# Kernel tuning notes

Measured on AMD Instinct MI355X. Metric: run time of the kernel, lower is better.

## Reference

```python
import jax, jax.numpy as jnp
import numpy as np
from jax import lax

D_MODEL = 512
N_BLOCKS = 8
VOCAB = 2048
MEL = 80
D_INNER = 2 * D_MODEL      # standard Mamba expand=2
STATE = 16                 # AudioConstants.MAMBA_STATE_DIM
DT_RANK = D_MODEL // 16    # 32
CONV_K = 4                 # causal depthwise conv kernel
B, T = 4, 2048


def setup_inputs() -> dict:
    key = jax.random.key(0)
    ks = jax.random.split(key, 16)
    s = 0.02
    nb = N_BLOCKS
    inp = {
        "feats": jax.random.normal(ks[0], (B, T, MEL), jnp.float32),
        "feat_lens": jax.random.randint(ks[1], (B,), 0, T, jnp.int32),
        # frontend
        "conv1_w": jax.random.normal(ks[2], (D_MODEL, MEL, 3), jnp.float32) * s,
        "conv1_b": jnp.zeros((D_MODEL,), jnp.float32),
        "conv2_w": jax.random.normal(ks[3], (D_MODEL, D_MODEL, 3), jnp.float32) * s,
        "conv2_b": jnp.zeros((D_MODEL,), jnp.float32),
        # stacked per-block Mamba params (leading dim = n_blocks)
        "norm_w": jnp.ones((nb, D_MODEL), jnp.float32),
        "in_proj_w": jax.random.normal(ks[4], (nb, D_MODEL, 2 * D_INNER), jnp.float32) * s,
        "dwconv_w": jax.random.normal(ks[5], (nb, D_INNER, CONV_K), jnp.float32) * s,
        "dwconv_b": jnp.zeros((nb, D_INNER), jnp.float32),
        "x_proj_w": jax.random.normal(ks[6], (nb, D_INNER, DT_RANK + 2 * STATE), jnp.float32) * s,
        "dt_proj_w": jax.random.normal(ks[7], (nb, DT_RANK, D_INNER), jnp.float32) * s,
        "dt_proj_b": jnp.full((nb, D_INNER), -4.6, jnp.float32),  # softplus(-4.6)~0.01
        "A_log": jnp.tile(jnp.log(jnp.arange(1, STATE + 1, dtype=jnp.float32))[None, None, :], (nb, D_INNER, 1)),
        "Dskip": jnp.ones((nb, D_INNER), jnp.float32),
        "out_proj_w": jax.random.normal(ks[8], (nb, D_INNER, D_MODEL), jnp.float32) * s,
        # CTC head
        "head_w": jax.random.normal(ks[9], (D_MODEL, VOCAB), jnp.float32) * s,
        "head_b": jnp.zeros((VOCAB,), jnp.float32),
    }
    return inp


def _conv1d(x, w, b, stride, pad):
    # x: (B, Cin, L), w: (Cout, Cin, K)
    y = lax.conv_general_dilated(x, w, (stride,), [(pad, pad)],
                                 dimension_numbers=("NCH", "OIH", "NCH"))
    return y + b[None, :, None]


def _mamba_layer(x, p):
    nw, ipw, cw, cb, xpw, dpw, dpb, alog, dsk, opw = p
    res = x
    # RMSNorm
    xn = x * lax.rsqrt(jnp.mean(x * x, axis=-1, keepdims=True) + 1e-5) * nw
    xz = xn @ ipw                                # (B, L, 2*di)
    xs, z = jnp.split(xz, 2, axis=-1)
    # causal depthwise conv over time
    xc = jnp.pad(xs.transpose(0, 2, 1), ((0, 0), (0, 0), (CONV_K - 1, 0)))
    xc = lax.conv_general_dilated(xc, cw[:, None, :], (1,), [(0, 0)],
                                  dimension_numbers=("NCH", "OIH", "NCH"),
                                  feature_group_count=D_INNER)
    xs = jax.nn.silu((xc + cb[None, :, None]).transpose(0, 2, 1))  # (B, L, di)
    # input-dependent SSM params
    xdb = xs @ xpw                               # (B, L, dt_rank + 2N)
    dt, Bm, Cm = jnp.split(xdb, [DT_RANK, DT_RANK + STATE], axis=-1)
    delta = jax.nn.softplus(dt @ dpw + dpb)      # (B, L, di)
    A = -jnp.exp(alog)                           # (di, N)
    dA = jnp.exp(delta[..., None] * A)           # (B, L, di, N)
    dBx = delta[..., None] * Bm[:, :, None, :] * xs[..., None]

    def step(h, inp):
        dA_t, dBx_t, C_t = inp                   # (B,di,N),(B,di,N),(B,N)
        h = dA_t * h + dBx_t
        y = jnp.einsum("bdn,bn->bd", h, C_t)
        return h, y

    h0 = jnp.zeros((x.shape[0], D_INNER, STATE), x.dtype)
    _, ys = lax.scan(step, h0, (dA.transpose(1, 0, 2, 3),
                                dBx.transpose(1, 0, 2, 3),
                                Cm.transpose(1, 0, 2)))
    y = ys.transpose(1, 0, 2) + xs * dsk          # (B, L, di)
    y = y * jax.nn.silu(z)
    return res + y @ opw, None


def reference(feats, feat_lens, conv1_w, conv1_b, conv2_w, conv2_b,
              norm_w, in_proj_w, dwconv_w, dwconv_b, x_proj_w,
              dt_proj_w, dt_proj_b, A_log, Dskip, out_proj_w,
              head_w, head_b):
    x = feats.transpose(0, 2, 1)                  # (B, 80, T)
    x = jax.nn.gelu(_conv1d(x, conv1_w, conv1_b, 2, 1), approximate=False)
    x = jax.nn.gelu(_conv1d(x, conv2_w, conv2_b, 2, 1), approximate=False)
    x = x.transpose(0, 2, 1)                      # (B, T/4, D)
    params = (norm_w, in_proj_w, dwconv_w, dwconv_b, x_proj_w,
              dt_proj_w, dt_proj_b, A_log, Dskip, out_proj_w)
    x, _ = lax.scan(_mamba_layer, x, params)
    logits = x @ head_w + head_b                  # (B, T/4, V)
    out_lens = jnp.maximum(feat_lens // 4, 1)
    return logits, out_lens
```

## Files before the change

kernel.cpp:

```cpp
#include <hip/hip_runtime.h>
#include <hip/hip_bf16.h>

#define DMODEL 512
#define NB 8
#define VOCABSZ 2048
#define MEL 80
#define DIN 1024
#define NSTATE 16
#define BATCH 4
#define TIN 2048
#define LL1 1024
#define LSEQ 512
#define MROWS (BATCH*LSEQ)
#define M1ROWS (BATCH*LL1)
#define NCHUNK 16
#define LCHUNK 32

typedef unsigned short u16;
typedef unsigned int   u32;
typedef __attribute__((ext_vector_type(8))) short short8;
typedef __attribute__((ext_vector_type(4))) float f32x4;

__device__ __forceinline__ float bf2f(u16 v) { return __uint_as_float(((u32)v) << 16); }
__device__ __forceinline__ u16 f2bf(float f) {
    u32 u = __float_as_uint(f);
    return (u16)((u + 0x7fffu + ((u >> 16) & 1u)) >> 16);
}
__device__ __forceinline__ float gelu_exact(float v) {
    return 0.5f * v * (1.0f + erff(v * 0.70710678118654752f));
}
__device__ __forceinline__ float silu_f(float v) { return v / (1.0f + __expf(-v)); }
__device__ __forceinline__ float softplus_f(float v) { return v > 20.f ? v : log1pf(__expf(v)); }

template<int WM, int WN, int MR, int NR, int EPI, int SPLITK>
__global__ __launch_bounds__(WM*WN*64) void gemm2_bf16(
    const u16* __restrict__ A, int lda,
    const u16* __restrict__ BT, int ldb,
    const float* __restrict__ bias,
    float* __restrict__ Cf, u16* __restrict__ Cb, int ldc,
    int K, int zstride)
{
    constexpr int BM = WM * MR * 16;
    constexpr int BN = WN * NR * 16;
    constexpr int NT = WM * WN * 64;
    constexpr int LA = (BM * 4) / NT;
    constexpr int LB = (BN * 4) / NT;
    __shared__ __align__(16) u16 As[2][BM * 32];
    __shared__ __align__(16) u16 Bs[2][BN * 32];
    const int tid = threadIdx.x;
    const int m0 = blockIdx.y * BM, n0 = blockIdx.x * BN;
    const int lane = tid & 63;
    const int wave = tid >> 6;
    const int wm = wave / WN, wn = wave % WN;
    const int lr = lane & 15, lk = lane >> 4;

    int kt0 = 0, kend = K;
    if (SPLITK > 1) {
        const int kb = K / SPLITK;
        kt0 = blockIdx.z * kb;
        kend = kt0 + kb;
        Cf += (size_t)blockIdx.z * zstride;
    }

    f32x4 acc[MR][NR];
#pragma unroll
    for (int m = 0; m < MR; ++m)
#pragma unroll
        for (int n = 0; n < NR; ++n) acc[m][n] = (f32x4){0.f, 0.f, 0.f, 0.f};

    auto stage = [&](int buf, int kt) {
#pragma unroll
        for (int c = 0; c < LA; ++c) {
            int idx = c * NT + tid;
            const u16* src = A + (size_t)(m0 + (idx >> 2)) * lda + kt + (idx & 3) * 8;
            __builtin_amdgcn_global_load_lds(
                (const __attribute__((address_space(1))) void*)src,
                (__attribute__((address_space(3))) void*)&As[buf][idx * 8], 16, 0, 0);
        }
#pragma unroll
        for (int c = 0; c < LB; ++c) {
            int idx = c * NT + tid;
            const u16* src = BT + (size_t)(n0 + (idx >> 2)) * ldb + kt + (idx & 3) * 8;
            __builtin_amdgcn_global_load_lds(
                (const __attribute__((address_space(1))) void*)src,
                (__attribute__((address_space(3))) void*)&Bs[buf][idx * 8], 16, 0, 0);
        }
    };

    stage(0, kt0);
    __syncthreads();
    int cur = 0;
    for (int kt = kt0; kt < kend; kt += 32) {
        if (kt + 32 < kend) stage(cur ^ 1, kt + 32);
        short8 a[MR], b[NR];
#pragma unroll
        for (int m = 0; m < MR; ++m)
            a[m] = *(const short8*)&As[cur][((wm * MR + m) * 16 + lr) * 32 + lk * 8];
#pragma unroll
        for (int n = 0; n < NR; ++n)
            b[n] = *(const short8*)&Bs[cur][((wn * NR + n) * 16 + lr) * 32 + lk * 8];
#pragma unroll
        for (int m = 0; m < MR; ++m)
#pragma unroll
            for (int n = 0; n < NR; ++n)
                acc[m][n] = __builtin_amdgcn_mfma_f32_16x16x32_bf16(a[m], b[n], acc[m][n], 0, 0, 0);
        __syncthreads();
        cur ^= 1;
    }

#pragma unroll
    for (int m = 0; m < MR; ++m) {
#pragma unroll
        for (int n = 0; n < NR; ++n) {
#pragma unroll
            for (int r = 0; r < 4; ++r) {
                const int row = m0 + (wm * MR + m) * 16 + lk * 4 + r;
                const int col = n0 + (wn * NR + n) * 16 + lr;
                float v = acc[m][n][r];
                if (EPI == 1)      v += bias[col];
                else if (EPI == 2) v = gelu_exact(v + bias[col]);
                else if (EPI == 3) v = softplus_f(v + bias[col]);
                else if (EPI == 4) v += Cf[(size_t)row * ldc + col];
                else if (EPI == 6) v *= bias[row];
                if (Cf) Cf[(size_t)row * ldc + col] = v;
                if (Cb) Cb[(size_t)row * ldc + col] = f2bf(v);
            }
        }
    }
}

__global__ __launch_bounds__(256) void tcast_k(const float* __restrict__ in, u16* __restrict__ out,
                                               int R, int C, size_t sin, size_t sout) {
    in  += (size_t)blockIdx.z * sin;
    out += (size_t)blockIdx.z * sout;
    __shared__ float s[32][33];
    const int tx = threadIdx.x & 31, ty = threadIdx.x >> 5;
    const int r0 = blockIdx.y * 32, c0 = blockIdx.x * 32;
#pragma unroll
    for (int i = 0; i < 4; ++i)
        s[ty + i * 8][tx] = in[(size_t)(r0 + ty + i * 8) * C + c0 + tx];
    __syncthreads();
#pragma unroll
    for (int i = 0; i < 4; ++i)
        out[(size_t)(c0 + ty + i * 8) * R + r0 + tx] = f2bf(s[tx][ty + i * 8]);
}

__global__ __launch_bounds__(256) void tcast_nw_k(const float* __restrict__ in, u16* __restrict__ out,
                                                  const float* __restrict__ nwp,
                                                  int R, int C, size_t sin, size_t sout, int nws) {
    in  += (size_t)blockIdx.z * sin;
    out += (size_t)blockIdx.z * sout;
    nwp += (size_t)blockIdx.z * nws;
    __shared__ float s[32][33];
    const int tx = threadIdx.x & 31, ty = threadIdx.x >> 5;
    const int r0 = blockIdx.y * 32, c0 = blockIdx.x * 32;
#pragma unroll
    for (int i = 0; i < 4; ++i)
        s[ty + i * 8][tx] = in[(size_t)(r0 + ty + i * 8) * C + c0 + tx];
    __syncthreads();
    const float nwv = nwp[r0 + tx];
#pragma unroll
    for (int i = 0; i < 4; ++i)
        out[(size_t)(c0 + ty + i * 8) * R + r0 + tx] = f2bf(s[tx][ty + i * 8] * nwv);
}

__global__ void castpad_k(const float* __restrict__ in, u16* __restrict__ out,
                          int rows, int cin, int cout, int instride,
                          size_t sin, size_t sout) {
    in  += (size_t)blockIdx.z * sin;
    out += (size_t)blockIdx.z * sout;
    int idx = blockIdx.x * 256 + threadIdx.x;
    if (idx >= rows * cout) return;
    int c = idx % cout, r = idx / cout;
    out[idx] = (c < cin) ? f2bf(in[(size_t)r * instride + c]) : (u16)0;
}

__global__ void im2col1_k(const float* __restrict__ feats, u16* __restrict__ out,
                          const int* __restrict__ feat_lens, float* __restrict__ lens_out) {
    int idx = blockIdx.x * 256 + threadIdx.x;
    if (blockIdx.x == 0 && threadIdx.x < BATCH) {
        int v = feat_lens[threadIdx.x] / 4;
        if (v < 1) v = 1;
        lens_out[threadIdx.x] = (float)v;
    }
    int c = idx & 255, m = idx >> 8;
    int l1 = m & (LL1 - 1), b = m >> 10;
    float v = 0.f;
    if (c < 240) {
        int ci = c / 3, kk = c - ci * 3;
        int t = 2 * l1 - 1 + kk;
        if (t >= 0 && t < TIN) v = feats[((size_t)b * TIN + t) * MEL + ci];
    }
    out[idx] = f2bf(v);
}

__global__ void im2col2_k(const u16* __restrict__ y1b, u16* __restrict__ out) {
    int idx = blockIdx.x * 256 + threadIdx.x;
    int c = idx % 1536, m = idx / 1536;
    int l = m & (LSEQ - 1), b = m >> 9;
    int ci = c / 3, kk = c - ci * 3;
    int t = 2 * l - 1 + kk;
    out[idx] = (t >= 0 && t < LL1) ? y1b[((size_t)b * LL1 + t) * 512 + ci] : (u16)0;
}

__global__ __launch_bounds__(256) void rowsc_k(const float* __restrict__ X,
                                               float* __restrict__ scrow) {
    const int lane = threadIdx.x & 63;
    const int row = blockIdx.x * 4 + (threadIdx.x >> 6);
    const float4 v0 = *(const float4*)&X[(size_t)row * 512 + lane * 8];
    const float4 v1 = *(const float4*)&X[(size_t)row * 512 + lane * 8 + 4];
    float ss = v0.x * v0.x + v0.y * v0.y + v0.z * v0.z + v0.w * v0.w
             + v1.x * v1.x + v1.y * v1.y + v1.z * v1.z + v1.w * v1.w;
#pragma unroll
    for (int o = 1; o < 64; o <<= 1) ss += __shfl_xor(ss, o);
    if (lane == 0) scrow[row] = rsqrtf(ss * (1.f / 512.f) + 1e-5f);
}

__global__ __launch_bounds__(256) void dwconv_silu_k(const u16* __restrict__ xzb,
                                                     const float* __restrict__ cw,
                                                     const float* __restrict__ cb,
                                                     u16* __restrict__ xsb) {
    int d = blockIdx.x * 256 + threadIdx.x;
    int m = blockIdx.y;
    int l = m & (LSEQ - 1);
    int b = m >> 9;
    float acc = cb[d];
    const float4 w4 = *reinterpret_cast<const float4*>(&cw[d * 4]);
    const float wk[4] = {w4.x, w4.y, w4.z, w4.w};
#pragma unroll
    for (int k = 0; k < 4; k++) {
        int t = l - 3 + k;
        if (t >= 0) acc += wk[k] * bf2f(xzb[((size_t)(b * LSEQ + t)) * (2 * DIN) + d]);
    }
    xsb[(size_t)m * DIN + d] = f2bf(silu_f(acc));
}

__global__ __launch_bounds__(256) void dtproj_k(
    const float* __restrict__ part, const u16* __restrict__ dpwT,
    const float* __restrict__ dpb, u16* __restrict__ delb)
{
    __shared__ __align__(16) u16 As[128 * 32];
    __shared__ __align__(16) u16 Bs[64 * 32];
    const int tid = threadIdx.x;
    const int m0 = blockIdx.y * 128, n0 = blockIdx.x * 64;
    {
        const int r = tid >> 1, hh = (tid & 1) * 16;
        const size_t o = (size_t)(m0 + r) * 64 + hh;
        float4 s[4];
#pragma unroll
        for (int q = 0; q < 4; ++q) {
            s[q] = *(const float4*)&part[o + q * 4];
#pragma unroll
            for (int p = 1; p < 4; ++p) {
                const float4 v = *(const float4*)&part[(size_t)p * 131072 + o + q * 4];
                s[q].x += v.x; s[q].y += v.y; s[q].z += v.z; s[q].w += v.w;
            }
        }
        u32 pk[8];
#pragma unroll
        for (int q = 0; q < 4; ++q) {
            pk[2 * q]     = (u32)f2bf(s[q].x) | ((u32)f2bf(s[q].y) << 16);
            pk[2 * q + 1] = (u32)f2bf(s[q].z) | ((u32)f2bf(s[q].w) << 16);
        }
        *(uint4*)&As[r * 32 + hh]     = make_uint4(pk[0], pk[1], pk[2], pk[3]);
        *(uint4*)&As[r * 32 + hh + 8] = make_uint4(pk[4], pk[5], pk[6], pk[7]);
    }
    {
        const int row = tid >> 2, p4 = (tid & 3) * 8;
        const u16* src = dpwT + (size_t)(n0 + row) * 32 + p4;
        __builtin_amdgcn_global_load_lds(
            (const __attribute__((address_space(1))) void*)src,
            (__attribute__((address_space(3))) void*)&Bs[row * 32 + p4], 16, 0, 0);
    }
    __syncthreads();
    const int lane = tid & 63, wave = tid >> 6;
    const int wm = wave >> 1, wn = wave & 1;
    const int lr = lane & 15, lk = lane >> 4;
    short8 b8[2];
#pragma unroll
    for (int n = 0; n < 2; ++n)
        b8[n] = *(const short8*)&Bs[((wn * 2 + n) * 16 + lr) * 32 + lk * 8];
#pragma unroll
    for (int m = 0; m < 4; ++m) {
        const short8 a8 = *(const short8*)&As[((wm * 4 + m) * 16 + lr) * 32 + lk * 8];
#pragma unroll
        for (int n = 0; n < 2; ++n) {
            f32x4 acc = __builtin_amdgcn_mfma_f32_16x16x32_bf16(a8, b8[n], (f32x4){0.f,0.f,0.f,0.f}, 0, 0, 0);
#pragma unroll
            for (int r = 0; r < 4; ++r) {
                const int row = m0 + (wm * 4 + m) * 16 + lk * 4 + r;
                const int col = n0 + (wn * 2 + n) * 16 + lr;
                delb[(size_t)row * DIN + col] = f2bf(softplus_f(acc[r] + dpb[col]));
            }
        }
    }
}

template<int PASS>
__global__ __launch_bounds__(256) void scan_chunk_k(
    const u16* __restrict__ deltab, const u16* __restrict__ xsb,
    const float* __restrict__ part, const u16* __restrict__ xzb,
    const float* __restrict__ alog, const float* __restrict__ dsk,
    float* __restrict__ P, float* __restrict__ Q,
    u16* __restrict__ yb)
{
    __shared__ float s_bc[LCHUNK * 32];
    __shared__ float s_dl[LCHUNK * 64];
    __shared__ float s_xs[LCHUNK * 64];
    __shared__ float s_z [PASS ? LCHUNK * 64 : 1];

    const int tid  = threadIdx.x;
    const int j    = tid & 3;
    const int dsub = tid >> 2;
    const int d0   = blockIdx.x * 64;
    const int c    = blockIdx.y;
    const int b    = blockIdx.z;
    const int d    = d0 + dsub;
    const size_t rbase = (size_t)b * LSEQ + c * LCHUNK;

    for (int idx = tid; idx < LCHUNK * 32; idx += 256) {
        int t = idx >> 5, cc = idx & 31;
        const size_t o = (rbase + t) * 64 + 32 + cc;
        s_bc[idx] = part[o] + part[131072 + o] + part[262144 + o] + part[393216 + o];
    }
    for (int idx = tid; idx < LCHUNK * 64; idx += 256) {
        int t = idx >> 6, dd = idx & 63;
        s_dl[idx] = bf2f(deltab[(rbase + t) * DIN + d0 + dd]);
        s_xs[idx] = bf2f(xsb[(rbase + t) * DIN + d0 + dd]);
        if (PASS) s_z[idx] = bf2f(xzb[(rbase + t) * (2 * DIN) + DIN + d0 + dd]);
    }
    __syncthreads();

    float a[4], h[4];
#pragma unroll
    for (int nj = 0; nj < 4; nj++)
        a[nj] = -__expf(alog[(size_t)d * NSTATE + j * 4 + nj]);

    const size_t chstride = (size_t)DIN * NSTATE;
    const size_t chcol = (size_t)d * NSTATE + j * 4;
    h[0] = h[1] = h[2] = h[3] = 0.f;
    if (PASS) {
        for (int c2 = 0; c2 < c; ++c2) {
            const size_t o = ((size_t)(b * NCHUNK + c2)) * chstride + chcol;
            const float4 Pv = *(const float4*)&P[o];
            const float4 Qv = *(const float4*)&Q[o];
            h[0] = fmaf(Pv.x, h[0], Qv.x);
            h[1] = fmaf(Pv.y, h[1], Qv.y);
            h[2] = fmaf(Pv.z, h[2], Qv.z);
            h[3] = fmaf(Pv.w, h[3], Qv.w);
        }
    }
    const float dskv = PASS ? dsk[d] : 0.f;
    float sdl = 0.f;

    for (int t = 0; t < LCHUNK; t++) {
        const float dl = s_dl[t * 64 + dsub];
        const float xv = s_xs[t * 64 + dsub];
        const float dlx = dl * xv;
        if (!PASS) sdl += dl;
        float yv = 0.f;
#pragma unroll
        for (int nj = 0; nj < 4; nj++) {
            const float bn = s_bc[t * 32 + j * 4 + nj];
            const float dA = __expf(dl * a[nj]);
            h[nj] = fmaf(dA, h[nj], dlx * bn);
            if (PASS) {
                const float cn = s_bc[t * 32 + 16 + j * 4 + nj];
                yv = fmaf(h[nj], cn, yv);
            }
        }
        if (PASS) {
            yv += __shfl_xor(yv, 1);
            yv += __shfl_xor(yv, 2);
            if (j == 0) {
                const float zv = s_z[t * 64 + dsub];
                yb[(rbase + t) * DIN + d] = f2bf((yv + xv * dskv) * silu_f(zv));
            }
        }
    }

    if (!PASS) {
        const size_t o = ((size_t)(b * NCHUNK + c)) * chstride + chcol;
        float4 Pv, Qv;
        Pv.x = __expf(a[0] * sdl); Pv.y = __expf(a[1] * sdl);
        Pv.z = __expf(a[2] * sdl); Pv.w = __expf(a[3] * sdl);
        Qv.x = h[0]; Qv.y = h[1]; Qv.z = h[2]; Qv.w = h[3];
        *(float4*)&P[o] = Pv;
        *(float4*)&Q[o] = Qv;
    }
}

extern "C" void kernel_launch(void* const* d_in, const int* in_sizes, int n_in,
                              void* d_out, int out_size, void* d_ws, size_t ws_size,
                              hipStream_t stream)
{
    const float* feats = (const float*)d_in[0];
    const int*   flens = (const int*)  d_in[1];
    const float* c1w = (const float*)d_in[2];
    const float* c1b = (const float*)d_in[3];
    const float* c2w = (const float*)d_in[4];
    const float* c2b = (const float*)d_in[5];
    const float* nw  = (const float*)d_in[6];
    const float* ipw = (const float*)d_in[7];
    const float* cw  = (const float*)d_in[8];
    const float* cb  = (const float*)d_in[9];
    const float* xpw = (const float*)d_in[10];
    const float* dpw = (const float*)d_in[11];
    const float* dpb = (const float*)d_in[12];
    const float* alog= (const float*)d_in[13];
    const float* dskp= (const float*)d_in[14];
    const float* opw = (const float*)d_in[15];
    const float* hw  = (const float*)d_in[16];
    const float* hb  = (const float*)d_in[17];

    float* ws = (float*)d_ws;
    u16*  XZb    = (u16*)ws;
    float* X     = ws + 2097152;
    u16*  Xb     = (u16*)(ws + 3145728);
    float* scrow = ws + 3670016;
    u16*  XSb    = (u16*)(ws + 4194304);
    u16*  DELb   = (u16*)(ws + 5242880);
    float* P     = ws + 6291456;
    u16*  Yb     = (u16*)(ws + 7340032);
    float* XDBp  = ws + 8388608;
    u16*  ipwTa  = (u16*)(ws + 10125312);
    u16*  opwTa  = (u16*)(ws + 14319616);
    u16*  hwT    = (u16*)(ws + 16416768);
    u16*  xpwT   = (u16*)(ws + 16941056);
    u16*  dpwT   = (u16*)(ws + 17203200);
    u16*  c1wb   = (u16*)(ws + 17334272);
    u16*  c2wb   = (u16*)(ws + 17399808);
    u16*  Y1b    = XSb;
    float* logits = (float*)d_out;
    float* Q     = logits;

    castpad_k<<<dim3(512, 1, 1), 256, 0, stream>>>(c1w, c1wb, 512, 240, 256, 240, 0, 0);
    castpad_k<<<dim3(3072, 1, 1), 256, 0, stream>>>(c2w, c2wb, 512, 1536, 1536, 1536, 0, 0);
    tcast_k<<<dim3(64, 16, 1), 256, 0, stream>>>(hw, hwT, 512, 2048, 0, 0);
    tcast_k<<<dim3(2, 32, 8), 256, 0, stream>>>(xpw, xpwT, 1024, 64, 65536, 65536);
    tcast_k<<<dim3(32, 1, 8), 256, 0, stream>>>(dpw, dpwT, 32, 1024, 32768, 32768);
    tcast_nw_k<<<dim3(64, 16, 8), 256, 0, stream>>>(ipw, ipwTa, nw, 512, 2048,
                                                    1048576, 1048576, DMODEL);
    tcast_k<<<dim3(16, 32, 8), 256, 0, stream>>>(opw, opwTa, 1024, 512, 524288, 524288);

    im2col1_k<<<4096, 256, 0, stream>>>(feats, XZb, flens, logits + (size_t)MROWS * VOCABSZ);
    gemm2_bf16<2, 2, 4, 2, 2, 1><<<dim3(8, 32), 256, 0, stream>>>(
        XZb, 256, c1wb, 256, c1b, nullptr, Y1b, 512, 256, 0);
    im2col2_k<<<12288, 256, 0, stream>>>(Y1b, XZb);
    gemm2_bf16<2, 2, 2, 2, 2, 1><<<dim3(8, 32), 256, 0, stream>>>(
        XZb, 1536, c2wb, 1536, c2b, X, Xb, 512, 1536, 0);

    for (int blk = 0; blk < NB; ++blk) {
        rowsc_k<<<512, 256, 0, stream>>>(X, scrow);
        gemm2_bf16<2, 2, 4, 2, 6, 1><<<dim3(32, 16), 256, 0, stream>>>(
            Xb, 512, ipwTa + (size_t)blk * 1048576, 512, scrow,
            nullptr, XZb, 2048, 512, 0);
        dwconv_silu_k<<<dim3(4, MROWS), 256, 0, stream>>>(
            XZb, cw + blk * DIN * 4, cb + blk * DIN, XSb);
        gemm2_bf16<2, 2, 2, 2, 0, 4><<<dim3(1, 32, 4), 256, 0, stream>>>(
            XSb, 1024, xpwT + (size_t)blk * 65536, 1024, nullptr,
            XDBp, nullptr, 64, 1024, 131072);
        dtproj_k<<<dim3(16, 16), 256, 0, stream>>>(
            XDBp, dpwT + (size_t)blk * 32768, dpb + blk * DIN, DELb);
        scan_chunk_k<0><<<dim3(16, NCHUNK, BATCH), 256, 0, stream>>>(
            DELb, XSb, XDBp, nullptr, alog + (size_t)blk * DIN * NSTATE,
            nullptr, P, Q, nullptr);
        scan_chunk_k<1><<<dim3(16, NCHUNK, BATCH), 256, 0, stream>>>(
            DELb, XSb, XDBp, XZb, alog + (size_t)blk * DIN * NSTATE,
            dskp + blk * DIN, P, Q, Yb);
        gemm2_bf16<2, 2, 2, 2, 4, 1><<<dim3(8, 32), 256, 0, stream>>>(
            Yb, 1024, opwTa + (size_t)blk * 524288, 1024, nullptr,
            X, Xb, 512, 1024, 0);
    }

    gemm2_bf16<2, 2, 4, 2, 1, 1><<<dim3(32, 16), 256, 0, stream>>>(
        Xb, 512, hwT, 512, hb, logits, nullptr, 2048, 512, 0);
}
```

Measured before the change: 863.6 us.

## Fuse RMSNorm row scale into in_proj GEMM and deepen K-tile to 64

Drops the separate rowsc_k kernel. The in_proj GEMM now accumulates sum of squares from the bf16 A tiles it already holds in registers, then applies rsqrt scaling in its epilogue through shared memory. All GEMMs also stage 64-wide K tiles (two 32-wide halves) per iteration, halving barrier count but doubling LDS use. The norm is now computed from the bf16 copy instead of the fp32 activations, which slightly changes numerics. Split-K is not used for in_proj, so every block still sees the full row.

```diff
diff --git a/kernel.cpp b/kernel.cpp
--- a/kernel.cpp
+++ b/kernel.cpp
@@ -33,7 +33,7 @@
 __device__ __forceinline__ float softplus_f(float v) { return v > 20.f ? v : log1pf(__expf(v)); }
 
 template<int WM, int WN, int MR, int NR, int EPI, int SPLITK>
-__global__ __launch_bounds__(WM*WN*64) void gemm2_bf16(
+__global__ __launch_bounds__(WM*WN*64) void gemm3_bf16(
     const u16* __restrict__ A, int lda,
     const u16* __restrict__ BT, int ldb,
     const float* __restrict__ bias,
@@ -45,8 +45,9 @@
     constexpr int NT = WM * WN * 64;
     constexpr int LA = (BM * 4) / NT;
     constexpr int LB = (BN * 4) / NT;
-    __shared__ __align__(16) u16 As[2][BM * 32];
-    __shared__ __align__(16) u16 Bs[2][BN * 32];
+    __shared__ __align__(16) u16 As[2][2 * BM * 32];
+    __shared__ __align__(16) u16 Bs[2][2 * BN * 32];
+    __shared__ float s_sc[EPI == 7 ? BM : 1];
     const int tid = threadIdx.x;
     const int m0 = blockIdx.y * BM, n0 = blockIdx.x * BN;
     const int lane = tid & 63;
@@ -67,61 +68,99 @@
     for (int m = 0; m < MR; ++m)
 #pragma unroll
         for (int n = 0; n < NR; ++n) acc[m][n] = (f32x4){0.f, 0.f, 0.f, 0.f};
+    float ssq[MR];
+#pragma unroll
+    for (int m = 0; m < MR; ++m) ssq[m] = 0.f;
 
     auto stage = [&](int buf, int kt) {
 #pragma unroll
-        for (int c = 0; c < LA; ++c) {
-            int idx = c * NT + tid;
-            const u16* src = A + (size_t)(m0 + (idx >> 2)) * lda + kt + (idx & 3) * 8;
-            __builtin_amdgcn_global_load_lds(
-                (const __attribute__((address_space(1))) void*)src,
-                (__attribute__((address_space(3))) void*)&As[buf][idx * 8], 16, 0, 0);
-        }
-#pragma unroll
-        for (int c = 0; c < LB; ++c) {
-            int idx = c * NT + tid;
-            const u16* src = BT + (size_t)(n0 + (idx >> 2)) * ldb + kt + (idx & 3) * 8;
-            __builtin_amdgcn_global_load_lds(
-                (const __attribute__((address_space(1))) void*)src,
-                (__attribute__((address_space(3))) void*)&Bs[buf][idx * 8], 16, 0, 0);
+        for (int h = 0; h < 2; ++h) {
+#pragma unroll
+            for (int c = 0; c < LA; ++c) {
+                int idx = c * NT + tid;
+                const u16* src = A + (size_t)(m0 + (idx >> 2)) * lda + kt + h * 32 + (idx & 3) * 8;
+                __builtin_amdgcn_global_load_lds(
+                    (const __attribute__((address_space(1))) void*)src,
+                    (__attribute__((address_space(3))) void*)&As[buf][h * BM * 32 + idx * 8], 16, 0, 0);
+            }
+#pragma unroll
+            for (int c = 0; c < LB; ++c) {
+                int idx = c * NT + tid;
+                const u16* src = BT + (size_t)(n0 + (idx >> 2)) * ldb + kt + h * 32 + (idx & 3) * 8;
+                __builtin_amdgcn_global_load_lds(
+                    (const __attribute__((address_space(1))) void*)src,
+                    (__attribute__((address_space(3))) void*)&Bs[buf][h * BN * 32 + idx * 8], 16, 0, 0);
+            }
         }
     };
 
     stage(0, kt0);
     __syncthreads();
     int cur = 0;
-    for (int kt = kt0; kt < kend; kt += 32) {
-        if (kt + 32 < kend) stage(cur ^ 1, kt + 32);
-        short8 a[MR], b[NR];
+    for (int kt = kt0; kt < kend; kt += 64) {
+        if (kt + 64 < kend) stage(cur ^ 1, kt + 64);
+        short8 a0[MR], a1[MR], b0[NR], b1[NR];
+#pragma unroll
+        for (int m = 0; m < MR; ++m) {
+            a0[m] = *(const short8*)&As[cur][((wm * MR + m) * 16 + lr) * 32 + lk * 8];
+            a1[m] = *(const short8*)&As[cur][BM * 32 + ((wm * MR + m) * 16 + lr) * 32 + lk * 8];
+        }
+#pragma unroll
+        for (int n = 0; n < NR; ++n) {
+            b0[n] = *(const short8*)&Bs[cur][((wn * NR + n) * 16 + lr) * 32 + lk * 8];
+            b1[n] = *(const short8*)&Bs[cur][BN * 32 + ((wn * NR + n) * 16 + lr) * 32 + lk * 8];
+        }
+        if (EPI == 7 && wn == 0) {
+#pragma unroll
+            for (int m = 0; m < MR; ++m)
+#pragma unroll
+                for (int j = 0; j < 8; ++j) {
+                    float v0 = bf2f((u16)a0[m][j]);
+                    float v1 = bf2f((u16)a1[m][j]);
+                    ssq[m] = fmaf(v0, v0, ssq[m]);
+                    ssq[m] = fmaf(v1, v1, ssq[m]);
+                }
+        }
 #pragma unroll
         for (int m = 0; m < MR; ++m)
-            a[m] = *(const short8*)&As[cur][((wm * MR + m) * 16 + lr) * 32 + lk * 8];
-#pragma unroll
-        for (int n = 0; n < NR; ++n)
-            b[n] = *(const short8*)&Bs[cur][((wn * NR + n) * 16 + lr) * 32 + lk * 8];
-#pragma unroll
-        for (int m = 0; m < MR; ++m)
-#pragma unroll
-            for (int n = 0; n < NR; ++n)
-                acc[m][n] = __builtin_amdgcn_mfma_f32_16x16x32_bf16(a[m], b[n], acc[m][n], 0, 0, 0);
+#pragma unroll
+            for (int n = 0; n < NR; ++n) {
+                acc[m][n] = __builtin_amdgcn_mfma_f32_16x16x32_bf16(a0[m], b0[n], acc[m][n], 0, 0, 0);
+                acc[m][n] = __builtin_amdgcn_mfma_f32_16x16x32_bf16(a1[m], b1[n], acc[m][n], 0, 0, 0);
+            }
         __syncthreads();
         cur ^= 1;
     }
 
+    if (EPI == 7) {
+        if (wn == 0) {
+#pragma unroll
+            for (int m = 0; m < MR; ++m) {
+                float ss = ssq[m];
+                ss += __shfl_xor(ss, 16);
+                ss += __shfl_xor(ss, 32);
+                if (lk == 0)
+                    s_sc[(wm * MR + m) * 16 + lr] = rsqrtf(ss * (1.f / 512.f) + 1e-5f);
+            }
+        }
+        __syncthreads();
+    }
+
 #pragma unroll
     for (int m = 0; m < MR; ++m) {
 #pragma unroll
         for (int n = 0; n < NR; ++n) {
 #pragma unroll
             for (int r = 0; r < 4; ++r) {
-                const int row = m0 + (wm * MR + m) * 16 + lk * 4 + r;
+                const int lrow = (wm * MR + m) * 16 + lk * 4 + r;
+                const int row = m0 + lrow;
                 const int col = n0 + (wn * NR + n) * 16 + lr;
                 float v = acc[m][n][r];
                 if (EPI == 1)      v += bias[col];
                 else if (EPI == 2) v = gelu_exact(v + bias[col]);
                 else if (EPI == 3) v = softplus_f(v + bias[col]);
                 else if (EPI == 4) v += Cf[(size_t)row * ldc + col];
-                else if (EPI == 6) v *= bias[row];
+                else if (EPI == 7) v *= s_sc[lrow];
                 if (Cf) Cf[(size_t)row * ldc + col] = v;
                 if (Cb) Cb[(size_t)row * ldc + col] = f2bf(v);
             }
@@ -201,19 +240,6 @@
     int ci = c / 3, kk = c - ci * 3;
     int t = 2 * l - 1 + kk;
     out[idx] = (t >= 0 && t < LL1) ? y1b[((size_t)b * LL1 + t) * 512 + ci] : (u16)0;
-}
-
-__global__ __launch_bounds__(256) void rowsc_k(const float* __restrict__ X,
-                                               float* __restrict__ scrow) {
-    const int lane = threadIdx.x & 63;
-    const int row = blockIdx.x * 4 + (threadIdx.x >> 6);
-    const float4 v0 = *(const float4*)&X[(size_t)row * 512 + lane * 8];
-    const float4 v1 = *(const float4*)&X[(size_t)row * 512 + lane * 8 + 4];
-    float ss = v0.x * v0.x + v0.y * v0.y + v0.z * v0.z + v0.w * v0.w
-             + v1.x * v1.x + v1.y * v1.y + v1.z * v1.z + v1.w * v1.w;
-#pragma unroll
-    for (int o = 1; o < 64; o <<= 1) ss += __shfl_xor(ss, o);
-    if (lane == 0) scrow[row] = rsqrtf(ss * (1.f / 512.f) + 1e-5f);
 }
 
 __global__ __launch_bounds__(256) void dwconv_silu_k(const u16* __restrict__ xzb,
@@ -417,7 +443,6 @@
     u16*  XZb    = (u16*)ws;
     float* X     = ws + 2097152;
     u16*  Xb     = (u16*)(ws + 3145728);
-    float* scrow = ws + 3670016;
     u16*  XSb    = (u16*)(ws + 4194304);
     u16*  DELb   = (u16*)(ws + 5242880);
     float* P     = ws + 6291456;
@@ -444,20 +469,19 @@
     tcast_k<<<dim3(16, 32, 8), 256, 0, stream>>>(opw, opwTa, 1024, 512, 524288, 524288);
 
     im2col1_k<<<4096, 256, 0, stream>>>(feats, XZb, flens, logits + (size_t)MROWS * VOCABSZ);
-    gemm2_bf16<2, 2, 4, 2, 2, 1><<<dim3(8, 32), 256, 0, stream>>>(
+    gemm3_bf16<2, 2, 4, 2, 2, 1><<<dim3(8, 32), 256, 0, stream>>>(
         XZb, 256, c1wb, 256, c1b, nullptr, Y1b, 512, 256, 0);
     im2col2_k<<<12288, 256, 0, stream>>>(Y1b, XZb);
-    gemm2_bf16<2, 2, 2, 2, 2, 1><<<dim3(8, 32), 256, 0, stream>>>(
+    gemm3_bf16<2, 2, 2, 2, 2, 1><<<dim3(8, 32), 256, 0, stream>>>(
         XZb, 1536, c2wb, 1536, c2b, X, Xb, 512, 1536, 0);
 
     for (int blk = 0; blk < NB; ++blk) {
-        rowsc_k<<<512, 256, 0, stream>>>(X, scrow);
-        gemm2_bf16<2, 2, 4, 2, 6, 1><<<dim3(32, 16), 256, 0, stream>>>(
-            Xb, 512, ipwTa + (size_t)blk * 1048576, 512, scrow,
+        gemm3_bf16<2, 2, 4, 2, 7, 1><<<dim3(32, 16), 256, 0, stream>>>(
+            Xb, 512, ipwTa + (size_t)blk * 1048576, 512, nullptr,
             nullptr, XZb, 2048, 512, 0);
         dwconv_silu_k<<<dim3(4, MROWS), 256, 0, stream>>>(
             XZb, cw + blk * DIN * 4, cb + blk * DIN, XSb);
-        gemm2_bf16<2, 2, 2, 2, 0, 4><<<dim3(1, 32, 4), 256, 0, stream>>>(
+        gemm3_bf16<2, 2, 2, 2, 0, 4><<<dim3(1, 32, 4), 256, 0, stream>>>(
             XSb, 1024, xpwT + (size_t)blk * 65536, 1024, nullptr,
             XDBp, nullptr, 64, 1024, 131072);
         dtproj_k<<<dim3(16, 16), 256, 0, stream>>>(
@@ -468,11 +492,11 @@
         scan_chunk_k<1><<<dim3(16, NCHUNK, BATCH), 256, 0, stream>>>(
             DELb, XSb, XDBp, XZb, alog + (size_t)blk * DIN * NSTATE,
             dskp + blk * DIN, P, Q, Yb);
-        gemm2_bf16<2, 2, 2, 2, 4, 1><<<dim3(8, 32), 256, 0, stream>>>(
+        gemm3_bf16<2, 2, 2, 2, 4, 1><<<dim3(8, 32), 256, 0, stream>>>(
             Yb, 1024, opwTa + (size_t)blk * 524288, 1024, nullptr,
             X, Xb, 512, 1024, 0);
     }
 
-    gemm2_bf16<2, 2, 4, 2, 1, 1><<<dim3(32, 16), 256, 0, stream>>>(
+    gemm3_bf16<2, 2, 4, 2, 1, 1><<<dim3(32, 16), 256, 0, stream>>>(
         Xb, 512, hwT, 512, hb, logits, nullptr, 2048, 512, 0);
 }
```

After: 822.2 us. -4.8%, faster.
